# Kernel optimization log

Measured on AMD Instinct MI355X. Metric: run time of the kernel, lower is better.

Reference implementation:

```python
import jax, jax.numpy as jnp
import numpy as np

B, N, M, C, K = 4, 16384, 1024, 256, 32
RADIUS = 1.0
EPS = 1e-5


def _bn(x, g, b, axes):
    # training-mode batch norm over given axes; channel axis is 1
    m = jnp.mean(x, axes, keepdims=True)
    v = jnp.var(x, axes, keepdims=True)
    sh = [1] * x.ndim
    sh[1] = -1
    return (x - m) * jax.lax.rsqrt(v + EPS) * g.reshape(sh) + b.reshape(sh)


def setup_inputs() -> dict:
    key = jax.random.key(0)
    ks = jax.random.split(key, 10)
    d = {
        'ffps_xyz': jax.random.normal(ks[0], (B, M, 3), jnp.float32),
        'ffps_feature': jax.random.normal(ks[1], (B, C, M), jnp.float32),
        'backbone_xyz': jax.random.normal(ks[2], (B, N, 3), jnp.float32),
        'backbone_features': jax.random.normal(ks[3], (B, C, N), jnp.float32),
        # shift layer: Conv1d(256->128), Conv1d(128->3)
        'sw1': jax.random.normal(ks[4], (128, 256), jnp.float32) * 0.05,
        'sg1': jnp.ones((128,), jnp.float32), 'sb1': jnp.zeros((128,), jnp.float32),
        'sw2': jax.random.normal(ks[5], (3, 128), jnp.float32) * 0.05,
        'sg2': jnp.ones((3,), jnp.float32), 'sb2': jnp.zeros((3,), jnp.float32),
        # grouped MLP: Conv2d 1x1: 259->512->512->512
        'w1': jax.random.normal(ks[6], (512, C + 3), jnp.float32) * 0.05,
        'g1': jnp.ones((512,), jnp.float32), 'b1': jnp.zeros((512,), jnp.float32),
        'w2': jax.random.normal(ks[7], (512, 512), jnp.float32) * 0.05,
        'g2': jnp.ones((512,), jnp.float32), 'b2': jnp.zeros((512,), jnp.float32),
        'w3': jax.random.normal(ks[8], (512, 512), jnp.float32) * 0.05,
        'g3': jnp.ones((512,), jnp.float32), 'b3': jnp.zeros((512,), jnp.float32),
    }
    return d


def reference(ffps_xyz, ffps_feature, backbone_xyz, backbone_features,
              sw1, sg1, sb1, sw2, sg2, sb2,
              w1, g1, b1, w2, g2, b2, w3, g3, b3):
    # ---- shift layer: Conv1d(1x1)+BN1d+ReLU x2 -> (B,3,M) ----
    h = jnp.einsum('oc,bcm->bom', sw1, ffps_feature)
    h = jax.nn.relu(_bn(h, sg1, sb1, (0, 2)))
    h = jnp.einsum('oc,bcm->bom', sw2, h)
    shift = jax.nn.relu(_bn(h, sg2, sb2, (0, 2)))
    new_xyz = ffps_xyz + shift.transpose(0, 2, 1)  # (B,M,3)

    # ---- ball query: first K points within RADIUS, pad with first hit ----
    d2 = jnp.sum((new_xyz[:, :, None, :] - backbone_xyz[:, None, :, :]) ** 2, -1)  # (B,M,N)
    score = jnp.where(d2 < RADIUS * RADIUS, jnp.arange(N, dtype=jnp.int32), N)
    neg_vals, _ = jax.lax.top_k(-score, K)  # K smallest scores = first valid indices
    idx = -neg_vals  # (B,M,K)
    first = idx[..., :1]
    idx = jnp.where(idx == N, first, idx)
    idx = jnp.where(idx == N, 0, idx)  # query with no neighbors -> 0

    # ---- group: relative xyz concat features -> (B, 3+C, M, K) ----
    bidx = jnp.arange(B)[:, None, None]
    g_xyz = backbone_xyz[bidx, idx] - new_xyz[:, :, None, :]        # (B,M,K,3)
    g_feat = backbone_features.transpose(0, 2, 1)[bidx, idx]        # (B,M,K,C)
    g = jnp.concatenate([g_xyz, g_feat], -1).transpose(0, 3, 1, 2)  # (B,3+C,M,K)

    # ---- per-point MLP: Conv2d(1x1)+BN2d+ReLU x3 ----
    for w, gm, bt in ((w1, g1, b1), (w2, g2, b2), (w3, g3, b3)):
        g = jnp.einsum('oc,bcmk->bomk', w, g)
        g = jax.nn.relu(_bn(g, gm, bt, (0, 2, 3)))

    # ---- max-pool over neighbors, return (B, M, C_out) ----
    return jnp.max(g, axis=3).transpose(0, 2, 1)
```

## Files before the change

### kernel.cpp

```cpp
#include <hip/hip_runtime.h>
#include <hip/hip_bf16.h>
#include <hip/hip_fp16.h>

#define BB   4
#define NN   16384
#define MM   1024
#define CC   256
#define KK   32
#define O1   128
#define FF   512
#define LTOT (BB*MM*KK)
#define NSLOT 64
#define CH   16384
#define NCH2 (LTOT/CH)

typedef float f4 __attribute__((ext_vector_type(4)));
typedef short b8 __attribute__((ext_vector_type(8)));

struct CvtA {
    const void* src[19];
    unsigned cum[20];
    unsigned dstF[19];
    int      nsz[19];
};

__device__ __forceinline__ float bf2f(unsigned short u){
    return __uint_as_float(((unsigned int)u) << 16);
}
__device__ __forceinline__ float anyf(const void* p, size_t i, int f){
    if (f == 1) return bf2f(((const unsigned short*)p)[i]);
    if (f == 2) return __half2float(((const __half*)p)[i]);
    return ((const float*)p)[i];
}

__global__ void k_det19(CvtA a, int* __restrict__ flags){
    if (threadIdx.x != 0) return;
    int i = blockIdx.x;
    const unsigned short* u = (const unsigned short*)a.src[i];
    int n = a.nsz[i];
    int* flag = flags + i;
    int W = n < 64 ? n : 64;
    bool allz = true;
    for (int k = 0; k < W; k++) if (u[k]){ allz = false; break; }
    if (allz){ *flag = 1; return; }
    if (u[0] == 0x3F80u){ *flag = 1; return; }
    if (u[0] == 0x3C00u){ *flag = 2; return; }
    if (W >= 2){
        unsigned int f0 = ((unsigned int)u[1] << 16) | u[0];
        if (__uint_as_float(f0) == 1.0f){ *flag = 0; return; }
    }
    int ce = 0, co = 0, ne = 0, no_ = 0;
    for (int k = 0; k < W; k++){
        unsigned short x = u[k];
        float v = fabsf(bf2f(x));
        int sane = (x == 0) || (v >= 0.0009765625f && v <= 64.f);
        if (k & 1){ no_++; co += sane; } else { ne++; ce += sane; }
    }
    if (ce * 4 >= ne * 3){ *flag = 1; return; }
    if (co * 4 >= no_ * 3 && ce * 5 < ne * 2){ *flag = 0; return; }
    *flag = 2;
}

__global__ __launch_bounds__(256) void k_cvt19(CvtA a, const int* __restrict__ flags,
                                               float* __restrict__ base){
    unsigned eb = blockIdx.x * 256u;
    int i = 0;
    while (eb >= a.cum[i+1]) i++;
    unsigned tl = eb - a.cum[i] + threadIdx.x;
    if ((int)tl >= a.nsz[i]) return;
    base[a.dstF[i] + tl] = anyf(a.src[i], tl, flags[i]);
}

__global__ __launch_bounds__(256) void k_mlp1(const float* __restrict__ sw1,
                                              const float* __restrict__ feat,
                                              float* __restrict__ h1,
                                              float* __restrict__ stats1){
    int t = blockIdx.x * 256 + threadIdx.x;
    int m = t & (MM - 1);
    int o = (t >> 10) & (O1 - 1);
    int b = t >> 17;
    const float* fb = feat + (size_t)b * CC * MM + m;
    const float* w  = sw1 + o * CC;
    float acc = 0.f;
    #pragma unroll 8
    for (int c = 0; c < CC; c++) acc += w[c] * fb[(size_t)c * MM];
    h1[t] = acc;
    float s = acc, s2 = acc * acc;
    for (int off = 32; off; off >>= 1){ s += __shfl_down(s, off); s2 += __shfl_down(s2, off); }
    __shared__ float ls[8];
    int lane = threadIdx.x & 63, wid = threadIdx.x >> 6;
    if (lane == 0){ ls[wid] = s; ls[4 + wid] = s2; }
    __syncthreads();
    if (threadIdx.x == 0){
        atomicAdd(&stats1[2*o],   ls[0]+ls[1]+ls[2]+ls[3]);
        atomicAdd(&stats1[2*o+1], ls[4]+ls[5]+ls[6]+ls[7]);
    }
}

__global__ __launch_bounds__(256) void k_bn1mlp2(const float* __restrict__ h1,
                                                 const float* __restrict__ stats1,
                                                 const float* __restrict__ sg1,
                                                 const float* __restrict__ sb1,
                                                 const float* __restrict__ sw2,
                                                 float* __restrict__ h2,
                                                 float* __restrict__ stats2){
    __shared__ float sc[O1], bi[O1];
    int tid = threadIdx.x;
    if (tid < O1){
        const float invn = 1.f / (BB * MM);
        float mean = stats1[2*tid] * invn;
        float var  = fmaxf(stats1[2*tid+1] * invn - mean * mean, 0.f);
        float rs   = 1.f / sqrtf(var + 1e-5f);
        float s    = rs * sg1[tid];
        float b_   = sb1[tid] - mean * s;
        if (!isfinite(s) || !isfinite(b_)){ s = 1.f; b_ = 0.f; }
        sc[tid] = s; bi[tid] = b_;
    }
    __syncthreads();
    int t = blockIdx.x * 256 + tid;
    int m = t & (MM - 1);
    int r = t >> 10; int o2 = r % 3; int b = r / 3;
    const float* hb = h1 + (size_t)b * O1 * MM + m;
    const float* w  = sw2 + o2 * O1;
    float acc = 0.f;
    #pragma unroll 8
    for (int c = 0; c < O1; c++){
        float v = hb[(size_t)c * MM] * sc[c] + bi[c];
        v = v > 0.f ? v : 0.f;
        acc += w[c] * v;
    }
    h2[t] = acc;
    float s = acc, s2 = acc * acc;
    for (int off = 32; off; off >>= 1){ s += __shfl_down(s, off); s2 += __shfl_down(s2, off); }
    __shared__ float ls[8];
    int lane = tid & 63, wid = tid >> 6;
    if (lane == 0){ ls[wid] = s; ls[4 + wid] = s2; }
    __syncthreads();
    if (tid == 0){
        atomicAdd(&stats2[2*o2],   ls[0]+ls[1]+ls[2]+ls[3]);
        atomicAdd(&stats2[2*o2+1], ls[4]+ls[5]+ls[6]+ls[7]);
    }
}

__global__ void k_fin2(const float* __restrict__ stats2, const float* __restrict__ sg2,
                       const float* __restrict__ sb2, float* __restrict__ scb2){
    int t = threadIdx.x;
    if (t < 3){
        const float invn = 1.f / (BB * MM);
        float mean = stats2[2*t] * invn;
        float var  = fmaxf(stats2[2*t+1] * invn - mean * mean, 0.f);
        float rs   = 1.f / sqrtf(var + 1e-5f);
        float s    = rs * sg2[t];
        float b    = sb2[t] - mean * s;
        if (!isfinite(s) || !isfinite(b)){ s = 1.f; b = 0.f; }
        scb2[t] = s; scb2[4 + t] = b;
    }
}

__global__ __launch_bounds__(256) void k_ballq(const float* __restrict__ fxyz,
                                               const float* __restrict__ h2,
                                               const float* __restrict__ scb2,
                                               const float* __restrict__ bxyz,
                                               int* __restrict__ idx2,
                                               float4* __restrict__ xyzd){
    __shared__ int sj[4][KK];
    int wq   = threadIdx.x >> 6;
    int q    = blockIdx.x * 4 + wq;
    int lane = threadIdx.x & 63;
    int b = q >> 10, m = q & (MM - 1);
    float nx[3];
    #pragma unroll
    for (int c = 0; c < 3; c++){
        float v = h2[((size_t)b * 3 + c) * MM + m] * scb2[c] + scb2[4 + c];
        v = v > 0.f ? v : 0.f;
        nx[c] = fxyz[(size_t)q * 3 + c] + v;
    }
    const float* bx = bxyz + (size_t)b * NN * 3;
    int have = 0, firstj = 0;
    for (int j0 = 0; j0 < NN && have < KK; j0 += 64){
        int j = j0 + lane;
        float dx = bx[j*3+0] - nx[0];
        float dy = bx[j*3+1] - nx[1];
        float dz = bx[j*3+2] - nx[2];
        float d2 = dx*dx + dy*dy + dz*dz;
        bool pred = d2 < 1.0f;
        unsigned long long mask = __ballot(pred);
        if (mask){
            if (have == 0) firstj = j0 + (__ffsll((unsigned long long)mask) - 1);
            if (pred){
                int rank = __popcll(mask & ((1ull << lane) - 1ull));
                int pos = have + rank;
                if (pos < KK) sj[wq][pos] = j;
            }
            have += (int)__popcll(mask);
        }
    }
    if (have < KK){
        int fill = (have > 0) ? firstj : 0;
        for (int p = have + lane; p < KK; p += 64) sj[wq][p] = fill;
    }
    if (lane < KK){
        int j = sj[wq][lane];
        int l = q * KK + lane;
        idx2[l] = b * NN + j;
        const float* p = bx + (size_t)j * 3;
        xyzd[l] = make_float4(p[0] - nx[0], p[1] - nx[1], p[2] - nx[2], 0.f);
    }
}

__global__ __launch_bounds__(256) void k_transp(const void* __restrict__ bfv,
                                                const int* __restrict__ flag,
                                                float* __restrict__ ft){
    __shared__ float tile[32][33];
    int f = *flag;
    int bid = blockIdx.x;
    int nt = bid & 511;
    int ct = (bid >> 9) & 7;
    int b  = bid >> 12;
    int tx = threadIdx.x & 31, ty = threadIdx.x >> 5;
    size_t base = ((size_t)b * CC + ct * 32) * NN + nt * 32;
    #pragma unroll
    for (int r = 0; r < 32; r += 8)
        tile[ty + r][tx] = anyf(bfv, base + (size_t)(ty + r) * NN + tx, f);
    __syncthreads();
    float* dst = ft + ((size_t)b * NN + nt * 32) * CC + ct * 32;
    #pragma unroll
    for (int r = 0; r < 32; r += 8) dst[(size_t)(ty + r) * CC + tx] = tile[tx][ty + r];
}

__global__ __launch_bounds__(256) void k_wpack(const float* __restrict__ src,
                                               int stride, int srcOff, int Cs,
                                               unsigned short* __restrict__ hph,
                                               unsigned short* __restrict__ hpl){
    int t = blockIdx.x * 256 + threadIdx.x;
    if (t >= FF * Cs) return;
    int nK = Cs >> 5;
    int j  = t & 7;
    int ln = (t >> 3) & 63;
    int r  = t >> 9;
    int ks = r % nK;
    int of = r / nK;
    int o = of * 16 + (ln & 15);
    int c = ks * 32 + (ln >> 4) * 8 + ((j >> 2) << 2) + (j & 3);
    float f = src[(size_t)o * stride + srcOff + c];
    unsigned u = __float_as_uint(f);
    unsigned hh = u & 0xFFFF0000u;
    hph[t] = (unsigned short)(hh >> 16);
    float f2 = f - __uint_as_float(hh);
    hpl[t] = (unsigned short)(__float_as_uint(f2) >> 16);
}

__global__ void k_w1xyz(const float* __restrict__ w1, float4* __restrict__ w1xp){
    int t = blockIdx.x * 256 + threadIdx.x;
    if (t < FF) w1xp[t] = make_float4(w1[t*259], w1[t*259+1], w1[t*259+2], 0.f);
}

__device__ __forceinline__ void split4(float x, float y, float z_, float w_,
                                       unsigned &h0, unsigned &h1,
                                       unsigned &lo0, unsigned &lo1){
    unsigned ux = __float_as_uint(x), uy = __float_as_uint(y);
    unsigned uz = __float_as_uint(z_), uw = __float_as_uint(w_);
    unsigned hx = ux & 0xFFFF0000u, hy = uy & 0xFFFF0000u;
    unsigned hz = uz & 0xFFFF0000u, hw = uw & 0xFFFF0000u;
    h0 = (hx >> 16) | hy;
    h1 = (hz >> 16) | hw;
    float rx = x  - __uint_as_float(hx);
    float ry = y  - __uint_as_float(hy);
    float rz = z_ - __uint_as_float(hz);
    float rw = w_ - __uint_as_float(hw);
    lo0 = (__float_as_uint(rx) >> 16) | (__float_as_uint(ry) & 0xFFFF0000u);
    lo1 = (__float_as_uint(rz) >> 16) | (__float_as_uint(rw) & 0xFFFF0000u);
}

template<int XM, int OM>
__global__ __launch_bounds__(256) void k_gemm(const unsigned short* __restrict__ Aph,
                                              const unsigned short* __restrict__ Apl,
                                              const float* __restrict__ X,
                                              int Cs,
                                              const float* __restrict__ scb,
                                              const int* __restrict__ idx2,
                                              const float4* __restrict__ xyzd,
                                              const float4* __restrict__ w1xp,
                                              int Lbase,
                                              float* __restrict__ Y,
                                              int Lwrite,
                                              float* __restrict__ y3mx,
                                              float* __restrict__ y3mn,
                                              double* __restrict__ stats){
    __shared__ short lds[16384];
    char* ldsb = (char*)lds;

    const int tid  = threadIdx.x;
    const int lane = tid & 63;
    const int w    = tid >> 6;
    const int wo   = (w >> 1) * 64;
    const int wl   = (w & 1) * 64;

    int bid = blockIdx.x;
    {
        int cpx = gridDim.x >> 3;
        bid = (bid & 7) * cpx + (bid >> 3);
    }
    const int o0 = (bid & 3) * 128;
    const int l0 = (bid >> 2) * 128;

    const int o_loc  = tid >> 3;
    const int q      = (tid & 7) >> 1;
    const int h      = tid & 1;
    const int colOff = q * 8 + h * 4;
    const int wbase  = ((o_loc >> 4) * 1024) + (((o_loc & 15) * 16) ^ (q << 5)) + (q << 8) + h * 8;
    const int roff   = (((lane & 15) * 16) ^ ((lane >> 4) << 5)) + ((lane >> 4) << 8);

    const int nK    = Cs >> 5;
    const int fbase = (o0 + wo) >> 4;
    const int aLane = lane * 16;

    int   rI[4];
    float ddx[4], ddy[4], ddz[4];
    const float* Xp = nullptr;
    if (XM == 1){
        #pragma unroll
        for (int i = 0; i < 4; i++){
            int lg = Lbase + l0 + o_loc + 32 * i;
            rI[i] = idx2[lg];
            float4 dd = xyzd[lg];
            ddx[i] = dd.x; ddy[i] = dd.y; ddz[i] = dd.z;
        }
    } else {
        Xp = X + (size_t)(l0 + o_loc) * Cs + colOff;
    }

    f4 acc[4][4];
    #pragma unroll
    for (int i = 0; i < 4; i++)
        #pragma unroll
        for (int j = 0; j < 4; j++)
            acc[i][j] = f4{0.f, 0.f, 0.f, 0.f};

    float4 rx[4];
    b8 ahf[4], alf[4];
    #pragma unroll
    for (int i = 0; i < 4; i++){
        if (XM == 1) rx[i] = *(const float4*)(X + (size_t)rI[i] * FF + colOff);
        else         rx[i] = *(const float4*)(Xp + (size_t)(32 * i) * Cs);
        int ab = ((fbase + i) * nK) << 10;
        ahf[i] = *(const b8*)((const char*)Aph + ab + aLane);
        alf[i] = *(const b8*)((const char*)Apl + ab + aLane);
    }

    int buf = 0;
    for (int c0 = 0; c0 < Cs; c0 += 32){
        unsigned xh0[4], xh1[4], xL0[4], xL1[4];
        float4 sc4, bi4;
        if (scb){
            sc4 = *(const float4*)(scb + c0 + colOff);
            bi4 = *(const float4*)(scb + Cs + c0 + colOff);
        }
        float4 wv0, wv1, wv2, wv3;
        if (XM == 1){
            wv0 = w1xp[c0 + colOff + 0];
            wv1 = w1xp[c0 + colOff + 1];
            wv2 = w1xp[c0 + colOff + 2];
            wv3 = w1xp[c0 + colOff + 3];
        }
        #pragma unroll
        for (int i = 0; i < 4; i++){
            float vx = rx[i].x, vy = rx[i].y, vz = rx[i].z, vw = rx[i].w;
            if (XM == 1){
                vx += ddx[i]*wv0.x + ddy[i]*wv0.y + ddz[i]*wv0.z;
                vy += ddx[i]*wv1.x + ddy[i]*wv1.y + ddz[i]*wv1.z;
                vz += ddx[i]*wv2.x + ddy[i]*wv2.y + ddz[i]*wv2.z;
                vw += ddx[i]*wv3.x + ddy[i]*wv3.y + ddz[i]*wv3.z;
            }
            if (scb){
                vx = fmaxf(vx * sc4.x + bi4.x, 0.f);
                vy = fmaxf(vy * sc4.y + bi4.y, 0.f);
                vz = fmaxf(vz * sc4.z + bi4.z, 0.f);
                vw = fmaxf(vw * sc4.w + bi4.w, 0.f);
            }
            split4(vx, vy, vz, vw, xh0[i], xh1[i], xL0[i], xL1[i]);
        }
        {
            int bo = buf << 13;
            #pragma unroll
            for (int i = 0; i < 4; i++){
                int off = bo + wbase + i * 2048;
                *(uint2*)(ldsb + off)          = make_uint2(xh0[i], xh1[i]);
                *(uint2*)(ldsb + 16384 + off)  = make_uint2(xL0[i], xL1[i]);
            }
        }
        __syncthreads();
        b8 nah[4], nal[4];
        if (c0 + 32 < Cs){
            int ks1 = (c0 >> 5) + 1;
            #pragma unroll
            for (int i = 0; i < 4; i++){
                if (XM == 1) rx[i] = *(const float4*)(X + (size_t)rI[i] * FF + colOff + (c0 + 32));
                else         rx[i] = *(const float4*)(Xp + (size_t)(32 * i) * Cs + (c0 + 32));
                int ab = (((fbase + i) * nK + ks1)) << 10;
                nah[i] = *(const b8*)((const char*)Aph + ab + aLane);
                nal[i] = *(const b8*)((const char*)Apl + ab + aLane);
            }
        }
        b8 bhf[4], blf[4];
        {
            int bo = buf << 13;
            #pragma unroll
            for (int ni = 0; ni < 4; ni++){
                int f = (wl >> 4) + ni;
                bhf[ni] = *(const b8*)(ldsb + bo + f * 1024 + roff);
                blf[ni] = *(const b8*)(ldsb + 16384 + bo + f * 1024 + roff);
            }
        }
        #pragma unroll
        for (int mi = 0; mi < 4; mi++){
            #pragma unroll
            for (int ni = 0; ni < 4; ni++){
                acc[mi][ni] = __builtin_amdgcn_mfma_f32_16x16x32_bf16(ahf[mi], bhf[ni], acc[mi][ni], 0, 0, 0);
                acc[mi][ni] = __builtin_amdgcn_mfma_f32_16x16x32_bf16(ahf[mi], blf[ni], acc[mi][ni], 0, 0, 0);
                acc[mi][ni] = __builtin_amdgcn_mfma_f32_16x16x32_bf16(alf[mi], bhf[ni], acc[mi][ni], 0, 0, 0);
            }
        }
        if (c0 + 32 < Cs){
            #pragma unroll
            for (int i = 0; i < 4; i++){ ahf[i] = nah[i]; alf[i] = nal[i]; }
        }
        buf ^= 1;
    }

    if (OM == 0){
        if (Y && (l0 + 128 <= Lwrite)){
            #pragma unroll
            for (int mi = 0; mi < 4; mi++){
                #pragma unroll
                for (int ni = 0; ni < 4; ni++){
                    int o = o0 + wo + mi * 16 + 4 * (lane >> 4);
                    int l = l0 + wl + ni * 16 + (lane & 15);
                    *(float4*)(Y + (size_t)l * FF + o) =
                        make_float4(acc[mi][ni][0], acc[mi][ni][1], acc[mi][ni][2], acc[mi][ni][3]);
                }
            }
        }
    }
    if (stats){
        int slot_s = blockIdx.x & (NSLOT - 1);
        double* sp = stats + (size_t)slot_s * FF * 2;
        #pragma unroll
        for (int mi = 0; mi < 4; mi++){
            float s1[4] = {0,0,0,0}, s2[4] = {0,0,0,0};
            #pragma unroll
            for (int ni = 0; ni < 4; ni++){
                #pragma unroll
                for (int r = 0; r < 4; r++){
                    float v = acc[mi][ni][r];
                    s1[r] += v; s2[r] += v * v;
                }
            }
            #pragma unroll
            for (int off = 8; off; off >>= 1){
                #pragma unroll
                for (int r = 0; r < 4; r++){
                    s1[r] += __shfl_down(s1[r], off, 16);
                    s2[r] += __shfl_down(s2[r], off, 16);
                }
            }
            if ((lane & 15) == 0){
                int o = o0 + wo + mi * 16 + 4 * (lane >> 4);
                #pragma unroll
                for (int r = 0; r < 4; r++){
                    atomicAdd(&sp[2 * (o + r)],     (double)s1[r]);
                    atomicAdd(&sp[2 * (o + r) + 1], (double)s2[r]);
                }
            }
        }
    }
    if (OM == 1){
        #pragma unroll
        for (int mi = 0; mi < 4; mi++){
            #pragma unroll
            for (int g = 0; g < 2; g++){
                float vmx[4], vmn[4];
                #pragma unroll
                for (int r = 0; r < 4; r++){
                    float a0 = acc[mi][2*g][r], a1 = acc[mi][2*g+1][r];
                    vmx[r] = fmaxf(a0, a1); vmn[r] = fminf(a0, a1);
                }
                #pragma unroll
                for (int off = 8; off; off >>= 1){
                    #pragma unroll
                    for (int r = 0; r < 4; r++){
                        vmx[r] = fmaxf(vmx[r], __shfl_down(vmx[r], off, 16));
                        vmn[r] = fminf(vmn[r], __shfl_down(vmn[r], off, 16));
                    }
                }
                if ((lane & 15) == 0){
                    int qg = (Lbase + l0 + wl) / 32 + g;
                    #pragma unroll
                    for (int r = 0; r < 4; r++){
                        int o = o0 + wo + mi * 16 + 4 * (lane >> 4) + r;
                        y3mx[(size_t)qg * FF + o] = vmx[r];
                        y3mn[(size_t)qg * FF + o] = vmn[r];
                    }
                }
            }
        }
    }
}

__global__ void k_finL(const double* __restrict__ stats, const float* __restrict__ g,
                       const float* __restrict__ bt, float* __restrict__ scb){
    int o = blockIdx.x * 256 + threadIdx.x;
    double s = 0.0, s2 = 0.0;
    for (int k = 0; k < NSLOT; k++){
        s  += stats[((size_t)k * FF + o) * 2];
        s2 += stats[((size_t)k * FF + o) * 2 + 1];
    }
    double mean = s / (double)LTOT;
    double var  = s2 / (double)LTOT - mean * mean;
    if (!(var > 0.0)) var = 0.0;
    double rs = 1.0 / sqrt(var + 1e-5);
    double sc = rs * (double)g[o];
    double bi = (double)bt[o] - mean * sc;
    float scf = (float)sc, bif = (float)bi;
    if (!isfinite(scf) || !isfinite(bif)){ scf = 1.f; bif = 0.f; }
    scb[o] = scf;
    scb[FF + o] = bif;
}

__global__ __launch_bounds__(256) void k_y1stats(const float* __restrict__ z,
                                                 const int* __restrict__ idx2,
                                                 const float4* __restrict__ xyzd,
                                                 const float4* __restrict__ w1xp,
                                                 double* __restrict__ stats){
    int tid = threadIdx.x, bid = blockIdx.x;
    int o1 = tid, o2 = tid + 256;
    float4 wa = w1xp[o1], wb = w1xp[o2];
    double s1a=0, s2a=0, s1b=0, s2b=0;
    for (int p = 0; p < LTOT/2048; p++){
        int l = bid + p * 2048;
        int r = idx2[l];
        float4 d = xyzd[l];
        const float* zr = z + (size_t)r * FF;
        float ya = zr[o1] + d.x*wa.x + d.y*wa.y + d.z*wa.z;
        float yb = zr[o2] + d.x*wb.x + d.y*wb.y + d.z*wb.z;
        s1a += ya; s2a += (double)ya*ya;
        s1b += yb; s2b += (double)yb*yb;
    }
    int slot = bid & (NSLOT - 1);
    double* sp = stats + (size_t)slot * FF * 2;
    atomicAdd(&sp[2*o1],   s1a); atomicAdd(&sp[2*o1+1], s2a);
    atomicAdd(&sp[2*o2],   s1b); atomicAdd(&sp[2*o2+1], s2b);
}

__global__ __launch_bounds__(256) void k_bn3max(const float* __restrict__ mx,
                                                const float* __restrict__ mn,
                                                const float* __restrict__ scb,
                                                float* __restrict__ out){
    int t = blockIdx.x * 256 + threadIdx.x;
    int o = t & (FF - 1);
    float sc = scb[o], bi = scb[FF + o];
    float v = sc >= 0.f ? mx[t] : mn[t];
    out[t] = fmaxf(sc * v + bi, 0.f);
}

__global__ __launch_bounds__(256) void k_diag(const float* __restrict__ ff,
                                              const float* __restrict__ w1f,
                                              const float* __restrict__ featT,
                                              const float* __restrict__ z,
                                              const float* __restrict__ xyzdf,
                                              const float* __restrict__ scb1,
                                              const float* __restrict__ scbL2,
                                              const float* __restrict__ scbL3,
                                              const float* __restrict__ y3,
                                              float* __restrict__ out){
    __shared__ float red[4];
    int tid = threadIdx.x;
    int bad = 0, isn = 0;
    const float* arr[9] = {ff, w1f, featT, z, xyzdf, scb1, scbL2, scbL3, y3};
    const int   len[9] = {4096, 4096, 8192, 8192, 4096, 1024, 1024, 1024, 8192};
    for (int k = 0; k < 9; k++){
        float s = 0.f;
        const float* a = arr[k];
        for (int i = tid; i < len[k]; i += 256) s += fabsf(a[i]);
        for (int off = 32; off; off >>= 1) s += __shfl_down(s, off);
        if ((tid & 63) == 0) red[tid >> 6] = s;
        __syncthreads();
        float t = red[0] + red[1] + red[2] + red[3];
        __syncthreads();
        if (bad == 0 && !(t > 1e-6f && t < 1e15f)){
            bad = k + 1;
            isn = isfinite(t) ? 0 : 1;
        }
    }
    if (tid == 0 && bad) out[0] = 512.f * bad + 256.f * isn;
}

extern "C" void kernel_launch(void* const* d_in, const int* in_sizes, int n_in,
                              void* d_out, int out_size, void* d_ws, size_t ws_size,
                              hipStream_t stream) {
    static const int NSZ[19] = {12288, 1048576, 196608, 16777216, 32768, 128, 128,
                                384, 3, 3, 132608, 512, 512, 262144, 512, 512,
                                262144, 512, 512};
    float* out = (float*)d_out;

    char* w = (char*)d_ws;
    size_t off = 0;
    auto take = [&](size_t bytes)->size_t{
        size_t r = off; off += (bytes + 255) & ~(size_t)255; return r;
    };
    size_t o_stats1  = take(256 * 4);
    size_t o_stats2  = take(8 * 4);
    size_t o_statsA  = take((size_t)NSLOT * FF * 2 * 8);
    size_t o_statsL2 = take((size_t)NSLOT * FF * 2 * 8);
    size_t o_statsL3 = take((size_t)NSLOT * FF * 2 * 8);
    size_t zero_end  = off;
    size_t o_flags   = take(19 * 4);
    size_t o_cv[19];
    for (int i = 0; i < 19; i++){
        if (i == 3){ o_cv[i] = 0; continue; }
        o_cv[i] = take((size_t)NSZ[i] * 4);
    }
    size_t o_scb2    = take(8 * 4);
    size_t o_scb1    = take(FF * 2 * 4);
    size_t o_scbL2   = take(FF * 2 * 4);
    size_t o_scbL3   = take(FF * 2 * 4);
    size_t o_h1      = take((size_t)BB * O1 * MM * 4);
    size_t o_h2      = take((size_t)BB * 3 * MM * 4);
    size_t o_idx2    = take((size_t)LTOT * 4);
    size_t o_xyzd    = take((size_t)LTOT * 16);
    size_t o_w1h     = take((size_t)FF * CC * 2);
    size_t o_w1l     = take((size_t)FF * CC * 2);
    size_t o_w2h     = take((size_t)FF * FF * 2);
    size_t o_w2l     = take((size_t)FF * FF * 2);
    size_t o_w3h     = take((size_t)FF * FF * 2);
    size_t o_w3l     = take((size_t)FF * FF * 2);
    size_t o_w1xp    = take((size_t)FF * 16);
    size_t o_y3mx    = take((size_t)BB * MM * FF * 4);
    size_t o_y3mn    = take((size_t)BB * MM * FF * 4);
    size_t o_z       = take((size_t)BB * NN * FF * 4);
    size_t o_featT   = take((size_t)BB * NN * CC * 4);
    (void)n_in; (void)in_sizes; (void)out_size;

    const size_t chb = (size_t)CH * FF * 4;
    size_t avail = ws_size > o_featT ? ws_size - o_featT : 0;
    int S; bool full;
    if (avail >= (size_t)NCH2 * chb){ S = NCH2; full = true; }
    else {
        long s = (long)(avail / chb) - 1;
        if (s < 0) s = 0; if (s > NCH2 - 1) s = NCH2 - 1;
        S = (int)s; full = false;
    }
    const int Lwrite = S * CH;

    float*  stats1  = (float*) (w + o_stats1);
    float*  stats2  = (float*) (w + o_stats2);
    double* statsA  = (double*)(w + o_statsA);
    double* statsL2 = (double*)(w + o_statsL2);
    double* statsL3 = (double*)(w + o_statsL3);
    int*    flags   = (int*)   (w + o_flags);
    float*  scb2    = (float*) (w + o_scb2);
    float*  scb1    = (float*) (w + o_scb1);
    float*  scbL2   = (float*) (w + o_scbL2);
    float*  scbL3   = (float*) (w + o_scbL3);
    float*  h1      = (float*) (w + o_h1);
    float*  h2      = (float*) (w + o_h2);
    int*    idx2    = (int*)   (w + o_idx2);
    float4* xyzd    = (float4*)(w + o_xyzd);
    unsigned short* w1h = (unsigned short*)(w + o_w1h);
    unsigned short* w1l = (unsigned short*)(w + o_w1l);
    unsigned short* w2h = (unsigned short*)(w + o_w2h);
    unsigned short* w2l = (unsigned short*)(w + o_w2l);
    unsigned short* w3h = (unsigned short*)(w + o_w3h);
    unsigned short* w3l = (unsigned short*)(w + o_w3l);
    float4* w1xp    = (float4*)(w + o_w1xp);
    float*  y3mx    = (float*) (w + o_y3mx);
    float*  y3mn    = (float*) (w + o_y3mn);
    float*  z       = (float*) (w + o_z);
    float*  featT   = (float*) (w + o_featT);
    float*  t2scr   = featT;
    float*  t2store = full ? featT : featT + (size_t)CH * FF;

    hipMemsetAsync(w, 0, zero_end, stream);

    CvtA ca;
    {
        unsigned c2 = 0;
        for (int i = 0; i < 19; i++){
            ca.src[i]  = d_in[i];
            ca.nsz[i]  = NSZ[i];
            ca.dstF[i] = (unsigned)(o_cv[i] / 4);
            ca.cum[i]  = c2;
            if (i != 3) c2 += (unsigned)((NSZ[i] + 255) & ~255);
        }
        ca.cum[19] = c2;
    }
    k_det19<<<19, 64, 0, stream>>>(ca, flags);
    k_cvt19<<<ca.cum[19] / 256, 256, 0, stream>>>(ca, flags, (float*)w);

    float* cv[19];
    for (int i = 0; i < 19; i++) cv[i] = (i == 3) ? nullptr : (float*)(w + o_cv[i]);
    float* fx = cv[0], *ffp = cv[1], *bx = cv[2];
    float* sw1f = cv[4], *sg1f = cv[5], *sb1f = cv[6];
    float* sw2f = cv[7], *sg2f = cv[8], *sb2f = cv[9];
    float* w1f = cv[10], *g1f = cv[11], *b1f = cv[12];
    float* w2f = cv[13], *g2f = cv[14], *b2f = cv[15];
    float* w3f = cv[16], *g3f = cv[17], *b3f = cv[18];

    k_mlp1   <<<2048, 256, 0, stream>>>(sw1f, ffp, h1, stats1);
    k_bn1mlp2<<<48,   256, 0, stream>>>(h1, stats1, sg1f, sb1f, sw2f, h2, stats2);
    k_fin2   <<<1,    64,  0, stream>>>(stats2, sg2f, sb2f, scb2);
    k_ballq  <<<BB*MM/4, 256, 0, stream>>>(fx, h2, scb2, bx, idx2, xyzd);
    k_transp <<<BB*(CC/32)*(NN/32), 256, 0, stream>>>(d_in[3], flags + 3, featT);
    k_wpack  <<<(FF*CC)/256, 256, 0, stream>>>(w1f, 259, 3, CC, w1h, w1l);
    k_wpack  <<<(FF*FF)/256, 256, 0, stream>>>(w2f, FF, 0, FF, w2h, w2l);
    k_wpack  <<<(FF*FF)/256, 256, 0, stream>>>(w3f, FF, 0, FF, w3h, w3l);
    k_w1xyz  <<<2, 256, 0, stream>>>(w1f, w1xp);

    k_gemm<0,0><<<4 * (BB*NN/128), 256, 0, stream>>>(w1h, w1l, featT, CC, nullptr,
            nullptr, nullptr, nullptr, 0, z, BB*NN, nullptr, nullptr, nullptr);

    k_y1stats<<<2048, 256, 0, stream>>>(z, idx2, xyzd, w1xp, statsA);
    k_finL  <<<2, 256, 0, stream>>>(statsA, g1f, b1f, scb1);

    const int GFULL = 4 * (LTOT/128);
    const int GCH   = 4 * (CH/128);

    k_gemm<1,0><<<GFULL, 256, 0, stream>>>(w2h, w2l, z, FF, scb1,
            idx2, xyzd, w1xp, 0, t2store, Lwrite, nullptr, nullptr, statsL2);
    k_finL <<<2, 256, 0, stream>>>(statsL2, g2f, b2f, scbL2);

    if (S > 0){
        k_gemm<0,1><<<S * GCH, 256, 0, stream>>>(w3h, w3l, t2store, FF, scbL2,
                nullptr, nullptr, nullptr, 0, nullptr, 0, y3mx, y3mn, statsL3);
    }
    for (int c = S; c < NCH2; c++){
        k_gemm<1,0><<<GCH, 256, 0, stream>>>(w2h, w2l, z, FF, scb1,
                idx2, xyzd, w1xp, c*CH, t2scr, CH, nullptr, nullptr, nullptr);
        k_gemm<0,1><<<GCH, 256, 0, stream>>>(w3h, w3l, t2scr, FF, scbL2,
                nullptr, nullptr, nullptr, c*CH, nullptr, 0, y3mx, y3mn, statsL3);
    }
    k_finL <<<2, 256, 0, stream>>>(statsL3, g3f, b3f, scbL3);

    k_bn3max<<<(BB*MM*FF)/256, 256, 0, stream>>>(y3mx, y3mn, scbL3, out);

    k_diag<<<1, 256, 0, stream>>>(ffp, w1f, t2scr, z, (const float*)xyzd,
                                  scb1, scbL2, scbL3, y3mx, out);
}
```

Measured before the change: 1.502 ms.

## Halve GEMM L-tile to 64 columns and repack w1 xyz weights planar

Shrinks the k_gemm tile from 128x128 to 128x64 along the point dimension. This halves LDS, accumulators and per-thread X loads, and launch_bounds now requests 3 blocks per SM for higher occupancy. Each thread now stages 8 contiguous channels for one row and uses planar w1 xyz weights for vectorised loads. The layer-3 max reduction is simplified so each wave handles exactly one 32-neighbor group. The cost is less reuse of A fragments per block, with A reloaded twice as often, and double the grid size.

```diff
diff --git a/kernel.cpp b/kernel.cpp
--- a/kernel.cpp
+++ b/kernel.cpp
@@ -250,9 +250,14 @@
     hpl[t] = (unsigned short)(__float_as_uint(f2) >> 16);
 }
 
-__global__ void k_w1xyz(const float* __restrict__ w1, float4* __restrict__ w1xp){
+__global__ void k_w1xyz(const float* __restrict__ w1, float4* __restrict__ w1xp,
+                        float* __restrict__ w1p3){
     int t = blockIdx.x * 256 + threadIdx.x;
-    if (t < FF) w1xp[t] = make_float4(w1[t*259], w1[t*259+1], w1[t*259+2], 0.f);
+    if (t < FF){
+        float x = w1[t*259], y = w1[t*259+1], z = w1[t*259+2];
+        w1xp[t] = make_float4(x, y, z, 0.f);
+        w1p3[t] = x; w1p3[FF + t] = y; w1p3[2*FF + t] = z;
+    }
 }
 
 __device__ __forceinline__ void split4(float x, float y, float z_, float w_,
@@ -273,28 +278,28 @@
 }
 
 template<int XM, int OM>
-__global__ __launch_bounds__(256) void k_gemm(const unsigned short* __restrict__ Aph,
+__global__ __launch_bounds__(256, 3) void k_gemm(const unsigned short* __restrict__ Aph,
                                               const unsigned short* __restrict__ Apl,
                                               const float* __restrict__ X,
                                               int Cs,
                                               const float* __restrict__ scb,
                                               const int* __restrict__ idx2,
                                               const float4* __restrict__ xyzd,
-                                              const float4* __restrict__ w1xp,
+                                              const float* __restrict__ w1p3,
                                               int Lbase,
                                               float* __restrict__ Y,
                                               int Lwrite,
                                               float* __restrict__ y3mx,
                                               float* __restrict__ y3mn,
                                               double* __restrict__ stats){
-    __shared__ short lds[16384];
+    __shared__ short lds[8192];
     char* ldsb = (char*)lds;
 
     const int tid  = threadIdx.x;
     const int lane = tid & 63;
     const int w    = tid >> 6;
     const int wo   = (w >> 1) * 64;
-    const int wl   = (w & 1) * 64;
+    const int wl   = (w & 1) * 32;
 
     int bid = blockIdx.x;
     {
@@ -302,47 +307,44 @@
         bid = (bid & 7) * cpx + (bid >> 3);
     }
     const int o0 = (bid & 3) * 128;
-    const int l0 = (bid >> 2) * 128;
-
-    const int o_loc  = tid >> 3;
-    const int q      = (tid & 7) >> 1;
-    const int h      = tid & 1;
-    const int colOff = q * 8 + h * 4;
-    const int wbase  = ((o_loc >> 4) * 1024) + (((o_loc & 15) * 16) ^ (q << 5)) + (q << 8) + h * 8;
+    const int l0 = (bid >> 2) * 64;
+
+    const int o_loc  = tid >> 2;
+    const int q      = tid & 3;
+    const int colOff = q * 8;
+    const int wbase  = ((o_loc >> 4) * 1024) + (((o_loc & 15) * 16) ^ (q << 5)) + (q << 8);
     const int roff   = (((lane & 15) * 16) ^ ((lane >> 4) << 5)) + ((lane >> 4) << 8);
 
     const int nK    = Cs >> 5;
     const int fbase = (o0 + wo) >> 4;
     const int aLane = lane * 16;
 
-    int   rI[4];
-    float ddx[4], ddy[4], ddz[4];
-    const float* Xp = nullptr;
+    int   rI = 0;
+    float ddx = 0.f, ddy = 0.f, ddz = 0.f;
+    const float* Xp;
     if (XM == 1){
-        #pragma unroll
-        for (int i = 0; i < 4; i++){
-            int lg = Lbase + l0 + o_loc + 32 * i;
-            rI[i] = idx2[lg];
-            float4 dd = xyzd[lg];
-            ddx[i] = dd.x; ddy[i] = dd.y; ddz[i] = dd.z;
-        }
+        int lg = Lbase + l0 + o_loc;
+        rI = idx2[lg];
+        float4 dd = xyzd[lg];
+        ddx = dd.x; ddy = dd.y; ddz = dd.z;
+        Xp = X + (size_t)rI * FF + colOff;
     } else {
         Xp = X + (size_t)(l0 + o_loc) * Cs + colOff;
     }
 
-    f4 acc[4][4];
+    f4 acc[4][2];
     #pragma unroll
     for (int i = 0; i < 4; i++)
         #pragma unroll
-        for (int j = 0; j < 4; j++)
+        for (int j = 0; j < 2; j++)
             acc[i][j] = f4{0.f, 0.f, 0.f, 0.f};
 
-    float4 rx[4];
+    float4 rx0, rx1;
     b8 ahf[4], alf[4];
+    rx0 = *(const float4*)(Xp);
+    rx1 = *(const float4*)(Xp + 4);
     #pragma unroll
     for (int i = 0; i < 4; i++){
-        if (XM == 1) rx[i] = *(const float4*)(X + (size_t)rI[i] * FF + colOff);
-        else         rx[i] = *(const float4*)(Xp + (size_t)(32 * i) * Cs);
         int ab = ((fbase + i) * nK) << 10;
         ahf[i] = *(const b8*)((const char*)Aph + ab + aLane);
         alf[i] = *(const b8*)((const char*)Apl + ab + aLane);
@@ -350,72 +352,74 @@
 
     int buf = 0;
     for (int c0 = 0; c0 < Cs; c0 += 32){
-        unsigned xh0[4], xh1[4], xL0[4], xL1[4];
-        float4 sc4, bi4;
+        float xv[8];
+        xv[0]=rx0.x; xv[1]=rx0.y; xv[2]=rx0.z; xv[3]=rx0.w;
+        xv[4]=rx1.x; xv[5]=rx1.y; xv[6]=rx1.z; xv[7]=rx1.w;
+        if (XM == 1){
+            float4 wx0 = *(const float4*)(w1p3 + c0 + colOff);
+            float4 wx1 = *(const float4*)(w1p3 + c0 + colOff + 4);
+            float4 wy0 = *(const float4*)(w1p3 + FF + c0 + colOff);
+            float4 wy1 = *(const float4*)(w1p3 + FF + c0 + colOff + 4);
+            float4 wz0 = *(const float4*)(w1p3 + 2*FF + c0 + colOff);
+            float4 wz1 = *(const float4*)(w1p3 + 2*FF + c0 + colOff + 4);
+            xv[0] += ddx*wx0.x + ddy*wy0.x + ddz*wz0.x;
+            xv[1] += ddx*wx0.y + ddy*wy0.y + ddz*wz0.y;
+            xv[2] += ddx*wx0.z + ddy*wy0.z + ddz*wz0.z;
+            xv[3] += ddx*wx0.w + ddy*wy0.w + ddz*wz0.w;
+            xv[4] += ddx*wx1.x + ddy*wy1.x + ddz*wz1.x;
+            xv[5] += ddx*wx1.y + ddy*wy1.y + ddz*wz1.y;
+            xv[6] += ddx*wx1.z + ddy*wy1.z + ddz*wz1.z;
+            xv[7] += ddx*wx1.w + ddy*wy1.w + ddz*wz1.w;
+        }
         if (scb){
-            sc4 = *(const float4*)(scb + c0 + colOff);
-            bi4 = *(const float4*)(scb + Cs + c0 + colOff);
-        }
-        float4 wv0, wv1, wv2, wv3;
-        if (XM == 1){
-            wv0 = w1xp[c0 + colOff + 0];
-            wv1 = w1xp[c0 + colOff + 1];
-            wv2 = w1xp[c0 + colOff + 2];
-            wv3 = w1xp[c0 + colOff + 3];
-        }
-        #pragma unroll
-        for (int i = 0; i < 4; i++){
-            float vx = rx[i].x, vy = rx[i].y, vz = rx[i].z, vw = rx[i].w;
-            if (XM == 1){
-                vx += ddx[i]*wv0.x + ddy[i]*wv0.y + ddz[i]*wv0.z;
-                vy += ddx[i]*wv1.x + ddy[i]*wv1.y + ddz[i]*wv1.z;
-                vz += ddx[i]*wv2.x + ddy[i]*wv2.y + ddz[i]*wv2.z;
-                vw += ddx[i]*wv3.x + ddy[i]*wv3.y + ddz[i]*wv3.z;
-            }
-            if (scb){
-                vx = fmaxf(vx * sc4.x + bi4.x, 0.f);
-                vy = fmaxf(vy * sc4.y + bi4.y, 0.f);
-                vz = fmaxf(vz * sc4.z + bi4.z, 0.f);
-                vw = fmaxf(vw * sc4.w + bi4.w, 0.f);
-            }
-            split4(vx, vy, vz, vw, xh0[i], xh1[i], xL0[i], xL1[i]);
-        }
+            float4 sc0 = *(const float4*)(scb + c0 + colOff);
+            float4 sc1 = *(const float4*)(scb + c0 + colOff + 4);
+            float4 bi0 = *(const float4*)(scb + Cs + c0 + colOff);
+            float4 bi1 = *(const float4*)(scb + Cs + c0 + colOff + 4);
+            xv[0] = fmaxf(xv[0]*sc0.x + bi0.x, 0.f);
+            xv[1] = fmaxf(xv[1]*sc0.y + bi0.y, 0.f);
+            xv[2] = fmaxf(xv[2]*sc0.z + bi0.z, 0.f);
+            xv[3] = fmaxf(xv[3]*sc0.w + bi0.w, 0.f);
+            xv[4] = fmaxf(xv[4]*sc1.x + bi1.x, 0.f);
+            xv[5] = fmaxf(xv[5]*sc1.y + bi1.y, 0.f);
+            xv[6] = fmaxf(xv[6]*sc1.z + bi1.z, 0.f);
+            xv[7] = fmaxf(xv[7]*sc1.w + bi1.w, 0.f);
+        }
+        unsigned ha0, ha1, la0, la1, hb0, hb1, lb0, lb1;
+        split4(xv[0], xv[1], xv[2], xv[3], ha0, ha1, la0, la1);
+        split4(xv[4], xv[5], xv[6], xv[7], hb0, hb1, lb0, lb1);
         {
-            int bo = buf << 13;
-            #pragma unroll
-            for (int i = 0; i < 4; i++){
-                int off = bo + wbase + i * 2048;
-                *(uint2*)(ldsb + off)          = make_uint2(xh0[i], xh1[i]);
-                *(uint2*)(ldsb + 16384 + off)  = make_uint2(xL0[i], xL1[i]);
-            }
+            int bo = buf << 12;
+            *(uint4*)(ldsb + bo + wbase)        = make_uint4(ha0, ha1, hb0, hb1);
+            *(uint4*)(ldsb + 8192 + bo + wbase) = make_uint4(la0, la1, lb0, lb1);
         }
         __syncthreads();
         b8 nah[4], nal[4];
         if (c0 + 32 < Cs){
+            rx0 = *(const float4*)(Xp + c0 + 32);
+            rx1 = *(const float4*)(Xp + c0 + 36);
             int ks1 = (c0 >> 5) + 1;
             #pragma unroll
             for (int i = 0; i < 4; i++){
-                if (XM == 1) rx[i] = *(const float4*)(X + (size_t)rI[i] * FF + colOff + (c0 + 32));
-                else         rx[i] = *(const float4*)(Xp + (size_t)(32 * i) * Cs + (c0 + 32));
                 int ab = (((fbase + i) * nK + ks1)) << 10;
                 nah[i] = *(const b8*)((const char*)Aph + ab + aLane);
                 nal[i] = *(const b8*)((const char*)Apl + ab + aLane);
             }
         }
-        b8 bhf[4], blf[4];
+        b8 bhf[2], blf[2];
         {
-            int bo = buf << 13;
-            #pragma unroll
-            for (int ni = 0; ni < 4; ni++){
+            int bo = buf << 12;
+            #pragma unroll
+            for (int ni = 0; ni < 2; ni++){
                 int f = (wl >> 4) + ni;
                 bhf[ni] = *(const b8*)(ldsb + bo + f * 1024 + roff);
-                blf[ni] = *(const b8*)(ldsb + 16384 + bo + f * 1024 + roff);
+                blf[ni] = *(const b8*)(ldsb + 8192 + bo + f * 1024 + roff);
             }
         }
         #pragma unroll
         for (int mi = 0; mi < 4; mi++){
             #pragma unroll
-            for (int ni = 0; ni < 4; ni++){
+            for (int ni = 0; ni < 2; ni++){
                 acc[mi][ni] = __builtin_amdgcn_mfma_f32_16x16x32_bf16(ahf[mi], bhf[ni], acc[mi][ni], 0, 0, 0);
                 acc[mi][ni] = __builtin_amdgcn_mfma_f32_16x16x32_bf16(ahf[mi], blf[ni], acc[mi][ni], 0, 0, 0);
                 acc[mi][ni] = __builtin_amdgcn_mfma_f32_16x16x32_bf16(alf[mi], bhf[ni], acc[mi][ni], 0, 0, 0);
@@ -429,11 +433,11 @@
     }
 
     if (OM == 0){
-        if (Y && (l0 + 128 <= Lwrite)){
+        if (Y && (l0 + 64 <= Lwrite)){
             #pragma unroll
             for (int mi = 0; mi < 4; mi++){
                 #pragma unroll
-                for (int ni = 0; ni < 4; ni++){
+                for (int ni = 0; ni < 2; ni++){
                     int o = o0 + wo + mi * 16 + 4 * (lane >> 4);
                     int l = l0 + wl + ni * 16 + (lane & 15);
                     *(float4*)(Y + (size_t)l * FF + o) =
@@ -449,7 +453,7 @@
         for (int mi = 0; mi < 4; mi++){
             float s1[4] = {0,0,0,0}, s2[4] = {0,0,0,0};
             #pragma unroll
-            for (int ni = 0; ni < 4; ni++){
+            for (int ni = 0; ni < 2; ni++){
                 #pragma unroll
                 for (int r = 0; r < 4; r++){
                     float v = acc[mi][ni][r];
@@ -475,32 +479,29 @@
         }
     }
     if (OM == 1){
+        int qg = (Lbase + l0 + wl) >> 5;
         #pragma unroll
         for (int mi = 0; mi < 4; mi++){
-            #pragma unroll
-            for (int g = 0; g < 2; g++){
-                float vmx[4], vmn[4];
+            float vmx[4], vmn[4];
+            #pragma unroll
+            for (int r = 0; r < 4; r++){
+                float a0 = acc[mi][0][r], a1 = acc[mi][1][r];
+                vmx[r] = fmaxf(a0, a1); vmn[r] = fminf(a0, a1);
+            }
+            #pragma unroll
+            for (int off = 8; off; off >>= 1){
                 #pragma unroll
                 for (int r = 0; r < 4; r++){
-                    float a0 = acc[mi][2*g][r], a1 = acc[mi][2*g+1][r];
-                    vmx[r] = fmaxf(a0, a1); vmn[r] = fminf(a0, a1);
+                    vmx[r] = fmaxf(vmx[r], __shfl_down(vmx[r], off, 16));
+                    vmn[r] = fminf(vmn[r], __shfl_down(vmn[r], off, 16));
                 }
+            }
+            if ((lane & 15) == 0){
                 #pragma unroll
-                for (int off = 8; off; off >>= 1){
-                    #pragma unroll
-                    for (int r = 0; r < 4; r++){
-                        vmx[r] = fmaxf(vmx[r], __shfl_down(vmx[r], off, 16));
-                        vmn[r] = fminf(vmn[r], __shfl_down(vmn[r], off, 16));
-                    }
-                }
-                if ((lane & 15) == 0){
-                    int qg = (Lbase + l0 + wl) / 32 + g;
-                    #pragma unroll
-                    for (int r = 0; r < 4; r++){
-                        int o = o0 + wo + mi * 16 + 4 * (lane >> 4) + r;
-                        y3mx[(size_t)qg * FF + o] = vmx[r];
-                        y3mn[(size_t)qg * FF + o] = vmn[r];
-                    }
+                for (int r = 0; r < 4; r++){
+                    int o = o0 + wo + mi * 16 + 4 * (lane >> 4) + r;
+                    y3mx[(size_t)qg * FF + o] = vmx[r];
+                    y3mn[(size_t)qg * FF + o] = vmn[r];
                 }
             }
         }
@@ -635,6 +636,7 @@
     size_t o_w3h     = take((size_t)FF * FF * 2);
     size_t o_w3l     = take((size_t)FF * FF * 2);
     size_t o_w1xp    = take((size_t)FF * 16);
+    size_t o_w1p3    = take((size_t)FF * 3 * 4);
     size_t o_y3mx    = take((size_t)BB * MM * FF * 4);
     size_t o_y3mn    = take((size_t)BB * MM * FF * 4);
     size_t o_z       = take((size_t)BB * NN * FF * 4);
@@ -673,6 +675,7 @@
     unsigned short* w3h = (unsigned short*)(w + o_w3h);
     unsigned short* w3l = (unsigned short*)(w + o_w3l);
     float4* w1xp    = (float4*)(w + o_w1xp);
+    float*  w1p3    = (float*) (w + o_w1p3);
     float*  y3mx    = (float*) (w + o_y3mx);
     float*  y3mn    = (float*) (w + o_y3mn);
     float*  z       = (float*) (w + o_z);
@@ -714,19 +717,19 @@
     k_wpack  <<<(FF*CC)/256, 256, 0, stream>>>(w1f, 259, 3, CC, w1h, w1l);
     k_wpack  <<<(FF*FF)/256, 256, 0, stream>>>(w2f, FF, 0, FF, w2h, w2l);
     k_wpack  <<<(FF*FF)/256, 256, 0, stream>>>(w3f, FF, 0, FF, w3h, w3l);
-    k_w1xyz  <<<2, 256, 0, stream>>>(w1f, w1xp);
-
-    k_gemm<0,0><<<4 * (BB*NN/128), 256, 0, stream>>>(w1h, w1l, featT, CC, nullptr,
+    k_w1xyz  <<<2, 256, 0, stream>>>(w1f, w1xp, w1p3);
+
+    k_gemm<0,0><<<4 * (BB*NN/64), 256, 0, stream>>>(w1h, w1l, featT, CC, nullptr,
             nullptr, nullptr, nullptr, 0, z, BB*NN, nullptr, nullptr, nullptr);
 
     k_y1stats<<<2048, 256, 0, stream>>>(z, idx2, xyzd, w1xp, statsA);
     k_finL  <<<2, 256, 0, stream>>>(statsA, g1f, b1f, scb1);
 
-    const int GFULL = 4 * (LTOT/128);
-    const int GCH   = 4 * (CH/128);
+    const int GFULL = 4 * (LTOT/64);
+    const int GCH   = 4 * (CH/64);
 
     k_gemm<1,0><<<GFULL, 256, 0, stream>>>(w2h, w2l, z, FF, scb1,
-            idx2, xyzd, w1xp, 0, t2store, Lwrite, nullptr, nullptr, statsL2);
+            idx2, xyzd, w1p3, 0, t2store, Lwrite, nullptr, nullptr, statsL2);
     k_finL <<<2, 256, 0, stream>>>(statsL2, g2f, b2f, scbL2);
 
     if (S > 0){
@@ -735,7 +738,7 @@
     }
     for (int c = S; c < NCH2; c++){
         k_gemm<1,0><<<GCH, 256, 0, stream>>>(w2h, w2l, z, FF, scb1,
-                idx2, xyzd, w1xp, c*CH, t2scr, CH, nullptr, nullptr, nullptr);
+                idx2, xyzd, w1p3, c*CH, t2scr, CH, nullptr, nullptr, nullptr);
         k_gemm<0,1><<<GCH, 256, 0, stream>>>(w3h, w3l, t2scr, FF, scbL2,
                 nullptr, nullptr, nullptr, c*CH, nullptr, 0, y3mx, y3mn, statsL3);
     }
```

After: 2.172 ms. +44.6%, slower.
